# Optimization experiments

Hardware: AMD Instinct MI355X
Metric: run time of the kernel (lower is better)

Reference implementation:

```python
import jax, jax.numpy as jnp
import numpy as np

T, B, E, H = 2048, 2, 1024, 16
DH = E // H
SCALE = DH ** -0.5
NEG = jnp.finfo(jnp.float32).min


def setup_inputs() -> dict:
    key = jax.random.key(0)
    ks = jax.random.split(key, 10)
    s = 0.02
    query = jax.random.normal(ks[0], (T, B, E), dtype=jnp.float32)
    key_padding_mask = jax.random.randint(ks[1], (B, T), 0, 2).astype(bool)
    # causal additive mask, broadcastable over (bsz, heads, tgt, src)
    causal = jnp.triu(jnp.ones((T, T), dtype=bool), k=1)
    attn_mask = jnp.where(causal, NEG, 0.0).astype(jnp.float32)[None, None]
    Wq = jax.random.normal(ks[2], (E, E), jnp.float32) * s
    bq = jax.random.normal(ks[3], (E,), jnp.float32) * s
    Wk = jax.random.normal(ks[4], (E, E), jnp.float32) * s
    bk = jax.random.normal(ks[5], (E,), jnp.float32) * s
    Wv = jax.random.normal(ks[6], (E, E), jnp.float32) * s
    bv = jax.random.normal(ks[7], (E,), jnp.float32) * s
    Wo = jax.random.normal(ks[8], (E, E), jnp.float32) * s
    bo = jax.random.normal(ks[9], (E,), jnp.float32) * s
    return {"query": query, "key_padding_mask": key_padding_mask, "attn_mask": attn_mask,
            "Wq": Wq, "bq": bq, "Wk": Wk, "bk": bk, "Wv": Wv, "bv": bv, "Wo": Wo, "bo": bo}


def _heads(x):
    # [T, B, E] -> [B, H, T, DH]
    return x.reshape(T, B, H, DH).transpose(1, 2, 0, 3)


def reference(query, key_padding_mask, attn_mask, Wq, bq, Wk, bk, Wv, bv, Wo, bo):
    # projections (torch Linear: x @ W.T + b); q scaled as in module
    q = _heads((query @ Wq.T + bq) * SCALE)          # [B,H,T,DH]
    k = _heads(query @ Wk.T + bk)                    # [B,H,S,DH] (self-attn: S=T)
    v = _heads(query @ Wv.T + bv)
    scores = jnp.einsum('bhtd,bhsd->bhts', q, k)     # [B,H,T,S]
    scores = scores + attn_mask                      # additive causal mask
    # key_padding_mask True -> masked_fill with dtype min
    scores = jnp.where(key_padding_mask[:, None, None, :], NEG, scores)
    probs = jax.nn.softmax(scores, axis=-1)
    ctx = jnp.einsum('bhts,bhsd->bhtd', probs, v)    # [B,H,T,DH]
    ctx = ctx.transpose(2, 0, 1, 3).reshape(T, B, E) # back to [T,B,E]
    return ctx @ Wo.T + bo
```

## Files before the change

kernel.cpp:

```cpp
#include <hip/hip_runtime.h>
#include <hip/hip_bf16.h>
#include <stdint.h>

typedef unsigned short u16;
typedef uint32_t u32;
typedef unsigned long long u64;
typedef __attribute__((ext_vector_type(8))) short bf16x8;
typedef __attribute__((ext_vector_type(4))) float f32x4;
typedef __attribute__((ext_vector_type(16))) float f32x16;
typedef __attribute__((ext_vector_type(2))) unsigned int u32x2;
typedef __attribute__((ext_vector_type(4))) u32 u32x4;

#define T_SEQ 2048

__device__ __forceinline__ float bf2f(u16 u) {
  union { u32 i; float f; } v; v.i = ((u32)u) << 16; return v.f;
}
__device__ __forceinline__ u16 f2bf(float f) {
  union { float f; u32 i; } v; v.f = f;
  u32 u = v.i;
  return (u16)((u + 0x7fffu + ((u >> 16) & 1u)) >> 16);
}

#if __has_builtin(__builtin_amdgcn_exp2f)
#define EXP2F(x) __builtin_amdgcn_exp2f(x)
#else
#define EXP2F(x) exp2f(x)
#endif

__device__ __forceinline__ u32 permpack(float lo, float hi) {
#if __has_builtin(__builtin_amdgcn_perm)
  return __builtin_amdgcn_perm(__float_as_uint(hi), __float_as_uint(lo), 0x07060302u);
#else
  return (__float_as_uint(hi) & 0xFFFF0000u) | (__float_as_uint(lo) >> 16);
#endif
}

__device__ __forceinline__ void plswap(u32& a, u32& b) {
#if __has_builtin(__builtin_amdgcn_permlane32_swap)
  u32x2 r = __builtin_amdgcn_permlane32_swap(a, b, false, false);
  a = r[0]; b = r[1];
#else
  u32 ra = __shfl_xor(a, 32, 64), rb = __shfl_xor(b, 32, 64);
  const bool hi_ = (threadIdx.x & 32) != 0;
  u32 na = hi_ ? rb : a;
  u32 nb = hi_ ? b : ra;
  a = na; b = nb;
#endif
}
__device__ __forceinline__ float othhalf(float x, bool ishi) {
  u32 a = __float_as_uint(x), b = a;
  plswap(a, b);
  return __uint_as_float(ishi ? a : b);
}

__device__ __forceinline__ void gload_lds16(const void* g, void* l) {
  __builtin_amdgcn_global_load_lds(
      (const __attribute__((address_space(1))) void*)g,
      (__attribute__((address_space(3))) void*)l, 16, 0, 0);
}

__global__ __launch_bounds__(256) void cvt5_kernel(
    const float* __restrict__ qsrc, const float* __restrict__ w0,
    const float* __restrict__ w1, const float* __restrict__ w2,
    const float* __restrict__ w3, u16* __restrict__ qbf, u16* __restrict__ wbf) {
  const int bx = blockIdx.x;
  const float* src; u16* dst; int i;
  if (bx < 4096) {
    src = qsrc; dst = qbf; i = (bx*256 + threadIdx.x)*4;
  } else {
    int t = bx - 4096;
    int z = t >> 10;
    src = (z == 0) ? w0 : (z == 1) ? w1 : (z == 2) ? w2 : w3;
    dst = wbf + (size_t)z * 1048576;
    i = ((t & 1023)*256 + threadIdx.x)*4;
  }
  const float4 v = *(const float4*)(src + i);
  ushort4 o;
  o.x = f2bf(v.x); o.y = f2bf(v.y); o.z = f2bf(v.z); o.w = f2bf(v.w);
  *(ushort4*)(dst + i) = o;
}

__device__ __forceinline__ void gemm_core_128x128(
    f32x4 acc[2][4], const u16* __restrict__ A, const u16* __restrict__ Bw,
    int bm, int bn, u16* As, u16* Bs)
{
  const int tid = threadIdx.x;
  const int w = tid >> 6, lane = tid & 63, g = lane >> 4, c = lane & 15;
  const int wr = (w & 3) * 32, wc = (w >> 2) * 64;
  for (int k0 = 0; k0 < 1024; k0 += 64) {
    __syncthreads();
    #pragma unroll
    for (int is = 0; is < 2; ++is) {
      int o = (is*8 + w)*1024 + lane*16;
      int row = o >> 7, c16 = (o >> 4) & 7;
      gload_lds16(A + (size_t)(bm*128 + row)*1024 + k0 + (c16 ^ (row & 7))*8,
                  (char*)As + (is*8 + w)*1024);
    }
    #pragma unroll
    for (int is = 0; is < 2; ++is) {
      int o = (is*8 + w)*1024 + lane*16;
      int row = o >> 7, c16 = (o >> 4) & 7;
      gload_lds16(Bw + (size_t)(bn*128 + row)*1024 + k0 + (c16 ^ (row & 7))*8,
                  (char*)Bs + (is*8 + w)*1024);
    }
    __syncthreads();
    bf16x8 af[2][2], bfr[4][2];
    #pragma unroll
    for (int mf = 0; mf < 2; ++mf)
      #pragma unroll
      for (int kc = 0; kc < 2; ++kc) {
        int row = wr + mf*16 + c;
        int colb = kc*64 + g*16;
        af[mf][kc] = *(const bf16x8*)((const char*)As + row*128 + (colb ^ ((row & 7) << 4)));
      }
    #pragma unroll
    for (int nf = 0; nf < 4; ++nf)
      #pragma unroll
      for (int kc = 0; kc < 2; ++kc) {
        int row = wc + nf*16 + c;
        int colb = kc*64 + g*16;
        bfr[nf][kc] = *(const bf16x8*)((const char*)Bs + row*128 + (colb ^ ((row & 7) << 4)));
      }
    #pragma unroll
    for (int mf = 0; mf < 2; ++mf)
      #pragma unroll
      for (int nf = 0; nf < 4; ++nf)
        #pragma unroll
        for (int kc = 0; kc < 2; ++kc)
          acc[mf][nf] = __builtin_amdgcn_mfma_f32_16x16x32_bf16(
              af[mf][kc], bfr[nf][kc], acc[mf][nf], 0, 0, 0);
  }
}

__global__ __launch_bounds__(512, 2) void gemm_qkv(
    const u16* __restrict__ Abf, const u16* __restrict__ Wbf,
    const float* __restrict__ bq, const float* __restrict__ bk,
    const float* __restrict__ bv, u16* __restrict__ qkvh)
{
  __shared__ __align__(16) u16 As[128*64];
  __shared__ __align__(16) u16 Bs[128*64];
  f32x4 acc[2][4];
  #pragma unroll
  for (int mf = 0; mf < 2; ++mf)
    #pragma unroll
    for (int nf = 0; nf < 4; ++nf) acc[mf][nf] = (f32x4){0.f,0.f,0.f,0.f};
  const int bx = blockIdx.x;
  const int bm = (bx & 7) * 4 + (bx >> 3);
  gemm_core_128x128(acc, Abf, Wbf, bm, blockIdx.y, As, Bs);
  const int tid = threadIdx.x, w = tid >> 6, lane = tid & 63, g = lane >> 4, c = lane & 15;
  const int wr = (w & 3) * 32, wc = (w >> 2) * 64;
  #pragma unroll
  for (int mf = 0; mf < 2; ++mf)
    #pragma unroll
    for (int nf = 0; nf < 4; ++nf) {
      int col = blockIdx.y*128 + wc + nf*16 + c;
      int z = col >> 10, colz = col & 1023;
      const float* bias = (z == 0) ? bq : (z == 1) ? bk : bv;
      float bcol = bias[colz];
      float scl = (z == 0) ? 0.18033688011112043f : 1.0f;
      int h = colz >> 6, d = colz & 63;
      u16* dst = qkvh + (size_t)z * 4194304;
      #pragma unroll
      for (int r = 0; r < 4; ++r) {
        int row = bm*128 + wr + mf*16 + g*4 + r;
        int t = row >> 1, bb = row & 1;
        float v = (acc[mf][nf][r] + bcol) * scl;
        dst[(size_t)(bb*16 + h)*131072 + (size_t)t*64 + d] = f2bf(v);
      }
    }
}

__global__ __launch_bounds__(512, 2) void gemm_out(
    const u16* __restrict__ ctx2, const u16* __restrict__ Wobf,
    const float* __restrict__ bo, float* __restrict__ out)
{
  __shared__ __align__(16) u16 As[128*64];
  __shared__ __align__(16) u16 Bs[128*64];
  f32x4 acc[2][4];
  #pragma unroll
  for (int mf = 0; mf < 2; ++mf)
    #pragma unroll
    for (int nf = 0; nf < 4; ++nf) acc[mf][nf] = (f32x4){0.f,0.f,0.f,0.f};
  const int bx = blockIdx.x;
  const int bm = (bx & 7) * 4 + (bx >> 3);
  gemm_core_128x128(acc, ctx2, Wobf, bm, blockIdx.y, As, Bs);
  const int tid = threadIdx.x, w = tid >> 6, lane = tid & 63, g = lane >> 4, c = lane & 15;
  const int wr = (w & 3) * 32, wc = (w >> 2) * 64;
  #pragma unroll
  for (int mf = 0; mf < 2; ++mf)
    #pragma unroll
    for (int nf = 0; nf < 4; ++nf) {
      int col = blockIdx.y*128 + wc + nf*16 + c;
      float bcol = bo[col];
      #pragma unroll
      for (int r = 0; r < 4; ++r) {
        int row = bm*128 + wr + mf*16 + g*4 + r;
        out[(size_t)row*1024 + col] = acc[mf][nf][r] + bcol;
      }
    }
}

__global__ __launch_bounds__(256) void vtrans_kernel(const u16* __restrict__ Vh,
                                                     u16* __restrict__ Vt,
                                                     float* __restrict__ vs) {
  __shared__ u16 tile[64][72];
  const int bh = blockIdx.x >> 5, tc = blockIdx.x & 31;
  const int t0 = tc * 64;
  const int tid = threadIdx.x;
  {
    const int tl = tid >> 2, d0 = (tid & 3) * 16;
    const u16* src = Vh + (size_t)bh*131072 + (size_t)(t0 + tl)*64 + d0;
    bf16x8 a = *(const bf16x8*)src;
    bf16x8 b2 = *(const bf16x8*)(src + 8);
    #pragma unroll
    for (int j = 0; j < 8; ++j) {
      tile[d0 + j][tl] = (u16)a[j];
      tile[d0 + 8 + j][tl] = (u16)b2[j];
    }
  }
  __syncthreads();
  {
    const int d = tid >> 2, tq = (tid & 3) * 16;
    bf16x8 o0, o1;
    float s = 0.f;
    #pragma unroll
    for (int j = 0; j < 8; ++j) {
      u16 x0 = tile[d][tq + j], x1 = tile[d][tq + 8 + j];
      o0[j] = (short)x0; o1[j] = (short)x1;
      s += bf2f(x0) + bf2f(x1);
    }
    u16* dst = Vt + (size_t)bh*131072 + (size_t)d*2048 + t0 + tq;
    *(bf16x8*)dst = o0;
    *(bf16x8*)(dst + 8) = o1;
    s += __shfl_xor(s, 1, 64);
    s += __shfl_xor(s, 2, 64);
    if ((tid & 3) == 0) atomicAdd(&vs[bh*64 + d], s);
  }
}

#define ZERO16 (f32x16){0.f,0.f,0.f,0.f,0.f,0.f,0.f,0.f,0.f,0.f,0.f,0.f,0.f,0.f,0.f,0.f}
#define NEGINF (-__builtin_inff())

__device__ const unsigned char CTBL[40] = {
  60, 44, 28, 12, 57, 59, 52, 37,
  61, 45, 29, 42, 40, 56, 53, 38,
  62, 46, 24, 25, 41, 58, 54, 49,
  63,  8, 20, 21, 32, 34, 55, 51,
   0,  4, 16, 17, 33, 36, 48, 50 };

__device__ __forceinline__ int pctx_off(int k, int ch) {
  if (k < 8)  return (k - 4);
  if (k < 12) return 4 + (k - 8)*2 + (ch - 1);
  return 12 + (k - 12)*3 + (ch - 1);
}
__device__ __forceinline__ int pml_off(int k, int ch) {
  if (k < 8)  return (k - 4)*2 + ch;
  if (k < 12) return 8 + (k - 8)*3 + ch;
  return 20 + (k - 12)*4 + ch;
}

__global__ __launch_bounds__(256, 2) void flash_attn(
    const u16* __restrict__ Qh, const u16* __restrict__ Kh,
    const u16* __restrict__ Vt, const int* __restrict__ kpm,
    const float* __restrict__ vsum, u16* __restrict__ ctx2,
    u16* __restrict__ pctxA, u16* __restrict__ pctxB,
    float* __restrict__ pml)
{
  __shared__ __align__(16) u16 Kl[2][4096];
  __shared__ __align__(16) u16 Vl[2][4096];

  const int tid = threadIdx.x;
  const int w = tid >> 6, lane = tid & 63;
  const int l31 = lane & 31, hi = lane >> 5;

  const int id = blockIdx.x;
  const int xcd = id & 7, rest = id >> 3;
  const int bh = xcd * 4 + (rest & 3);
  const int cidx = rest >> 2;
  const int v_tbl = CTBL[cidx];
  const int k = v_tbl >> 2, ch = v_tbl & 3;
  const int NS = (k >> 2) + 1;
  const int nt = 2*k + 2;
  const int lo = (nt * ch) / NS, hicap = (nt * (ch + 1)) / NS;

  const int b = bh >> 4, h = bh & 15;
  const size_t hbase = (size_t)bh * 131072;
  const int q = 128*k + 32*w + l31;
  const int myNt = 2*k + 1 + (w >> 1);

  bf16x8 qfrag[4];
  #pragma unroll
  for (int kt = 0; kt < 4; ++kt)
    qfrag[kt] = *(const bf16x8*)(Qh + hbase + (size_t)q*64 + kt*16 + hi*8);

  {
    const int s0t = lo * 64;
    const int jb = (w & 1) * 4;
    if (w < 2) {
      #pragma unroll
      for (int is = 0; is < 4; ++is) {
        int o = (jb + is)*1024 + lane*16;
        int row = o >> 7, c16 = (o >> 4) & 7;
        gload_lds16(Kh + hbase + (size_t)(s0t + row)*64 + (c16 ^ (row & 7))*8,
                    (char*)Kl[0] + (jb + is)*1024);
      }
    } else {
      #pragma unroll
      for (int is = 0; is < 4; ++is) {
        int o = (jb + is)*1024 + lane*16;
        int row = o >> 7, c16 = (o >> 4) & 7;
        gload_lds16(Vt + hbase + (size_t)row*2048 + s0t + (c16 ^ (row & 7))*8,
                    (char*)Vl[0] + (jb + is)*1024);
      }
    }
  }
  int kpmv_cur = kpm[b*T_SEQ + lo*64 + lane];
  int kpmv_nxt = 0;
  __syncthreads();

  float mrow = NEGINF, lrow = 0.f;
  f32x16 cacc0 = ZERO16, cacc1 = ZERO16;

  for (int t = lo; t < hicap; ++t) {
    const int cur = (t - lo) & 1, nxt = cur ^ 1;
    const int s0 = t * 64;
    const bool notLast = (t + 1 < hicap);
    const bool diag = (t >= myNt - 1);

    if (notLast) {
      const int s0n = s0 + 64;
      const int jb = (w & 1) * 4;
      if (w < 2) {
        #pragma unroll
        for (int is = 0; is < 4; ++is) {
          int o = (jb + is)*1024 + lane*16;
          int row = o >> 7, c16 = (o >> 4) & 7;
          gload_lds16(Kh + hbase + (size_t)(s0n + row)*64 + (c16 ^ (row & 7))*8,
                      (char*)Kl[nxt] + (jb + is)*1024);
        }
      } else {
        #pragma unroll
        for (int is = 0; is < 4; ++is) {
          int o = (jb + is)*1024 + lane*16;
          int row = o >> 7, c16 = (o >> 4) & 7;
          gload_lds16(Vt + hbase + (size_t)row*2048 + s0n + (c16 ^ (row & 7))*8,
                      (char*)Vl[nxt] + (jb + is)*1024);
        }
      }
      kpmv_nxt = kpm[b*T_SEQ + s0n + lane];
    }

    u32 kill0 = 0, kill1 = 0;
    {
      const u64 mask = __ballot(kpmv_cur != 0);
      const u32 m0 = (u32)mask, m1 = (u32)(mask >> 32);
      const u64 m4 = mask >> 4;
      const u32 m4l = (u32)m4, m4h = (u32)(m4 >> 32);
      const u32 w0m = hi ? m4l : m0;
      const u32 w1m = hi ? m4h : m1;
      const int lim = q - s0 - 4*hi;
      #pragma unroll
      for (int m = 0; m < 4; ++m) {
        u32 nib0 = (w0m >> (m*8)) & 15u;
        u32 nib1 = (w1m >> (m*8)) & 15u;
        if (diag) {
          int t0c = lim - m*8;       int c0 = min(max(t0c + 1, 0), 4);
          int t1c = lim - 32 - m*8;  int c1 = min(max(t1c + 1, 0), 4);
          nib0 |= (0xFu << c0) & 0xFu;
          nib1 |= (0xFu << c1) & 0xFu;
        }
        kill0 |= nib0 << (m*4);
        kill1 |= nib1 << (m*4);
      }
    }
    f32x16 st0, st1;
    #pragma unroll
    for (int i = 0; i < 16; ++i) {
      st0[i] = ((kill0 >> i) & 1u) ? NEGINF : 0.f;
      st1[i] = ((kill1 >> i) & 1u) ? NEGINF : 0.f;
    }

    bf16x8 kreg[2][4], vf[2][4];
    #pragma unroll
    for (int sub = 0; sub < 2; ++sub)
      #pragma unroll
      for (int kt = 0; kt < 4; ++kt) {
        int row = sub*32 + l31;
        int colb = kt*32 + hi*16;
        kreg[sub][kt] = *(const bf16x8*)((const char*)Kl[cur] + row*128 + (colb ^ ((row & 7) << 4)));
        vf[sub][kt]   = *(const bf16x8*)((const char*)Vl[cur] + row*128 + (colb ^ ((row & 7) << 4)));
      }

    __builtin_amdgcn_s_setprio(1);
    #pragma unroll
    for (int kt = 0; kt < 4; ++kt) {
      st0 = __builtin_amdgcn_mfma_f32_32x32x16_bf16(kreg[0][kt], qfrag[kt], st0, 0, 0, 0);
      st1 = __builtin_amdgcn_mfma_f32_32x32x16_bf16(kreg[1][kt], qfrag[kt], st1, 0, 0, 0);
    }
    __builtin_amdgcn_s_setprio(0);

    {
      float t8[8];
      #pragma unroll
      for (int i = 0; i < 8; ++i)
        t8[i] = fmaxf(fmaxf(st0[i], st0[i+8]), fmaxf(st1[i], st1[i+8]));
      float t4a = fmaxf(t8[0], t8[4]), t4b = fmaxf(t8[1], t8[5]);
      float t4c = fmaxf(t8[2], t8[6]), t4d = fmaxf(t8[3], t8[7]);
      float rm = fmaxf(fmaxf(t4a, t4b), fmaxf(t4c, t4d));
      rm = fmaxf(rm, othhalf(rm, hi != 0));

      const bool need = (rm > mrow + 8.f) || (mrow < -1e30f);
      if (__any(need)) {
        const float mn = fmaxf(mrow, rm);
        const float sc = (mn < -1e30f) ? 1.f : EXP2F(mrow - mn);
        mrow = mn;
        lrow *= sc;
        #pragma unroll
        for (int i = 0; i < 16; ++i) { cacc0[i] *= sc; cacc1[i] *= sc; }
      }
      const bool dead = (mrow < -1e30f);
      float a0 = 0.f, a1 = 0.f, a2 = 0.f, a3 = 0.f;
      #pragma unroll
      for (int i = 0; i < 16; i += 4) {
        float p0 = dead ? 0.f : EXP2F(st0[i+0] - mrow); st0[i+0] = p0; a0 += p0;
        float p1 = dead ? 0.f : EXP2F(st0[i+1] - mrow); st0[i+1] = p1; a1 += p1;
        float p2 = dead ? 0.f : EXP2F(st0[i+2] - mrow); st0[i+2] = p2; a2 += p2;
        float p3 = dead ? 0.f : EXP2F(st0[i+3] - mrow); st0[i+3] = p3; a3 += p3;
      }
      #pragma unroll
      for (int i = 0; i < 16; i += 4) {
        float p0 = dead ? 0.f : EXP2F(st1[i+0] - mrow); st1[i+0] = p0; a0 += p0;
        float p1 = dead ? 0.f : EXP2F(st1[i+1] - mrow); st1[i+1] = p1; a1 += p1;
        float p2 = dead ? 0.f : EXP2F(st1[i+2] - mrow); st1[i+2] = p2; a2 += p2;
        float p3 = dead ? 0.f : EXP2F(st1[i+3] - mrow); st1[i+3] = p3; a3 += p3;
      }
      float ps = (a0 + a1) + (a2 + a3);
      ps += othhalf(ps, hi != 0);
      lrow += ps;
    }

    u32 pk[8][2];
    #pragma unroll
    for (int m = 0; m < 4; ++m) {
      pk[m][0]   = permpack(st0[m*4+0], st0[m*4+1]);
      pk[m][1]   = permpack(st0[m*4+2], st0[m*4+3]);
      pk[4+m][0] = permpack(st1[m*4+0], st1[m*4+1]);
      pk[4+m][1] = permpack(st1[m*4+2], st1[m*4+3]);
    }
    bf16x8 pf[4];
    #pragma unroll
    for (int ks = 0; ks < 4; ++ks) {
      u32 w0p = pk[2*ks][0], w2p = pk[2*ks+1][0];
      u32 w1p = pk[2*ks][1], w3p = pk[2*ks+1][1];
      plswap(w0p, w2p);
      plswap(w1p, w3p);
      u32x4 wv = {w0p, w1p, w2p, w3p};
      pf[ks] = __builtin_bit_cast(bf16x8, wv);
    }

    __builtin_amdgcn_s_setprio(1);
    #pragma unroll
    for (int ks = 0; ks < 4; ++ks)
      cacc0 = __builtin_amdgcn_mfma_f32_32x32x16_bf16(vf[0][ks], pf[ks], cacc0, 0, 0, 0);
    #pragma unroll
    for (int ks = 0; ks < 4; ++ks)
      cacc1 = __builtin_amdgcn_mfma_f32_32x32x16_bf16(vf[1][ks], pf[ks], cacc1, 0, 0, 0);
    __builtin_amdgcn_s_setprio(0);

    kpmv_cur = kpmv_nxt;
    if (notLast) __syncthreads();
  }

  if (NS == 1) {
    const bool dead = (lrow == 0.f);
    const float rl = dead ? 0.f : 1.f / lrow;
    #pragma unroll
    for (int subd = 0; subd < 2; ++subd) {
      #pragma unroll
      for (int m = 0; m < 4; ++m) {
        const int d0 = subd*32 + hi*4 + m*8;
        float v0 = (subd ? cacc1[m*4+0] : cacc0[m*4+0]) * rl;
        float v1 = (subd ? cacc1[m*4+1] : cacc0[m*4+1]) * rl;
        float v2 = (subd ? cacc1[m*4+2] : cacc0[m*4+2]) * rl;
        float v3 = (subd ? cacc1[m*4+3] : cacc0[m*4+3]) * rl;
        if (dead) {
          const float* vs = vsum + bh*64 + d0;
          v0 = vs[0] * (1.0f/2048.0f);
          v1 = vs[1] * (1.0f/2048.0f);
          v2 = vs[2] * (1.0f/2048.0f);
          v3 = vs[3] * (1.0f/2048.0f);
        }
        ushort4 o;
        o.x = f2bf(v0); o.y = f2bf(v1); o.z = f2bf(v2); o.w = f2bf(v3);
        *(ushort4*)(ctx2 + (size_t)(q*2 + b)*1024 + h*64 + d0) = o;
      }
    }
  } else {
    const int row = w*32 + l31;
    if (!hi) {
      float2 ml; ml.x = mrow; ml.y = lrow;
      *(float2*)(pml + (size_t)(bh*36 + pml_off(k, ch))*256 + row*2) = ml;
    }
    u16* pc;
    if (ch == 0) {
      pc = ctx2 + (size_t)(q*2 + b)*1024 + h*64;
    } else {
      const int slot = bh*24 + pctx_off(k, ch);
      pc = (slot < 512) ? (pctxA + (size_t)slot*8192)
                        : (pctxB + (size_t)(slot - 512)*8192);
      pc += (size_t)row*64;
    }
    #pragma unroll
    for (int subd = 0; subd < 2; ++subd) {
      #pragma unroll
      for (int m = 0; m < 4; ++m) {
        const int d0 = subd*32 + hi*4 + m*8;
        const f32x16& cc = subd ? cacc1 : cacc0;
        ushort4 o;
        o.x = f2bf(cc[m*4+0]); o.y = f2bf(cc[m*4+1]);
        o.z = f2bf(cc[m*4+2]); o.w = f2bf(cc[m*4+3]);
        *(ushort4*)(pc + d0) = o;
      }
    }
  }
}

__global__ __launch_bounds__(256) void combine_kernel(
    const u16* __restrict__ pctxA, const u16* __restrict__ pctxB,
    const float* __restrict__ pml, const float* __restrict__ vsum,
    u16* __restrict__ ctx2)
{
  const int k = 4 + blockIdx.x;
  const int bh = blockIdx.y;
  const int NS = (k >> 2) + 1;
  const int b = bh >> 4, h = bh & 15;
  const int tid = threadIdx.x;
  const int row = tid >> 1, dh = (tid & 1) * 32;
  const int q = k*128 + row;

  const float* mlb = pml + (size_t)(bh*36 + pml_off(k, 0))*256 + row*2;
  float m0v = mlb[0],        l0v = mlb[1];
  float m1v = mlb[256+0],    l1v = mlb[256+1];
  float m2v = NEGINF, l2v = 0.f, m3v = NEGINF, l3v = 0.f;
  if (NS > 2) { m2v = mlb[512+0];  l2v = mlb[512+1]; }
  if (NS > 3) { m3v = mlb[768+0];  l3v = mlb[768+1]; }
  float ms = fmaxf(fmaxf(m0v, m1v), fmaxf(m2v, m3v));
  bool dead = (ms < -1e30f);
  const float w0 = dead ? 0.f : EXP2F(m0v - ms);
  const float w1 = dead ? 0.f : EXP2F(m1v - ms);
  const float w2 = (dead || NS <= 2) ? 0.f : EXP2F(m2v - ms);
  const float w3 = (dead || NS <= 3) ? 0.f : EXP2F(m3v - ms);
  const float lt = w0*l0v + w1*l1v + w2*l2v + w3*l3v;
  dead = dead || (lt == 0.f);
  const float rl = dead ? 0.f : 1.f / lt;

  u16* dst = ctx2 + (size_t)(q*2 + b)*1024 + h*64 + dh;
  const u16* pc1; const u16* pc2 = nullptr; const u16* pc3 = nullptr;
  {
    const int s1 = bh*24 + pctx_off(k, 1);
    pc1 = ((s1 < 512) ? (pctxA + (size_t)s1*8192) : (pctxB + (size_t)(s1-512)*8192))
          + (size_t)row*64 + dh;
    if (NS > 2) {
      const int s2 = bh*24 + pctx_off(k, 2);
      pc2 = ((s2 < 512) ? (pctxA + (size_t)s2*8192) : (pctxB + (size_t)(s2-512)*8192))
            + (size_t)row*64 + dh;
    }
    if (NS > 3) {
      const int s3 = bh*24 + pctx_off(k, 3);
      pc3 = ((s3 < 512) ? (pctxA + (size_t)s3*8192) : (pctxB + (size_t)(s3-512)*8192))
            + (size_t)row*64 + dh;
    }
  }
  #pragma unroll
  for (int g2 = 0; g2 < 4; ++g2) {
    bf16x8 a0 = *(const bf16x8*)(dst + g2*8);
    bf16x8 a1 = *(const bf16x8*)(pc1 + g2*8);
    bf16x8 o;
    #pragma unroll
    for (int j = 0; j < 8; ++j) {
      float v = w0*bf2f((u16)a0[j]) + w1*bf2f((u16)a1[j]);
      if (NS > 2) v += w2*bf2f((u16)((const u16*)pc2)[g2*8 + j]);
      if (NS > 3) v += w3*bf2f((u16)((const u16*)pc3)[g2*8 + j]);
      v *= rl;
      if (dead) v = vsum[bh*64 + dh + g2*8 + j] * (1.0f/2048.0f);
      o[j] = (short)f2bf(v);
    }
    *(bf16x8*)(dst + g2*8) = o;
  }
}

extern "C" void kernel_launch(void* const* d_in, const int* in_sizes, int n_in,
                              void* d_out, int out_size, void* d_ws, size_t ws_size,
                              hipStream_t stream) {
  const float* query = (const float*)d_in[0];
  const int*   kpm   = (const int*)d_in[1];
  const float* Wq = (const float*)d_in[3];
  const float* bq = (const float*)d_in[4];
  const float* Wk = (const float*)d_in[5];
  const float* bk = (const float*)d_in[6];
  const float* Wv = (const float*)d_in[7];
  const float* bv = (const float*)d_in[8];
  const float* Wo = (const float*)d_in[9];
  const float* bo = (const float*)d_in[10];

  char* ws = (char*)d_ws;
  u16*   qbf   = (u16*)(ws);
  u16*   Vt    = (u16*)(ws);
  u16*   wbf   = (u16*)(ws + 8388608);
  u16*   pctxB = (u16*)(ws + 8388608);
  u16*   qkvh  = (u16*)(ws + 16777216);
  u16*   pctxA = (u16*)(ws + 33554432);
  u16*   ctx2  = (u16*)(ws + 41943040);
  float* vsum  = (float*)(ws + 50331648);
  float* pml   = (float*)(ws + 50339840);

  cvt5_kernel<<<dim3(8192), 256, 0, stream>>>(query, Wq, Wk, Wv, Wo, qbf, wbf);

  hipMemsetAsync(vsum, 0, 2048 * sizeof(float), stream);

  gemm_qkv<<<dim3(32, 24), 512, 0, stream>>>(qbf, wbf, bq, bk, bv, qkvh);
  vtrans_kernel<<<dim3(1024), 256, 0, stream>>>(qkvh + 2*4194304, Vt, vsum);
  flash_attn<<<dim3(1280), 256, 0, stream>>>(qkvh, qkvh + 1*4194304,
                                             Vt, kpm, vsum, ctx2, pctxA, pctxB, pml);
  combine_kernel<<<dim3(12, 32), 256, 0, stream>>>(pctxA, pctxB, pml, vsum, ctx2);
  gemm_out<<<dim3(32, 8), 512, 0, stream>>>(ctx2, wbf + 3*1048576, bo, (float*)d_out);
}
```

Before: 141.8 us.

## Deepen flash-attention K/V prefetch to two tiles and precompute padding-mask bitmasks

The attention loop now keeps two K/V tiles in flight. It prefetches tile t+2 into the buffer just consumed and waits with explicit vmcnt counts and raw barriers instead of a full __syncthreads after issuing loads. The key-padding mask is packed into 64-bit ballot words by an extra block in the conversion kernel, so each attention iteration reads one u64 instead of a per-lane int load plus a ballot. This aims to hide global-load latency more fully and drop per-tile mask work. It relies on precise hand-written waitcnt values, which is fragile if the compiler reorders or adds memory ops.

```diff
diff --git a/kernel.cpp b/kernel.cpp
--- a/kernel.cpp
+++ b/kernel.cpp
@@ -63,8 +63,18 @@
 __global__ __launch_bounds__(256) void cvt5_kernel(
     const float* __restrict__ qsrc, const float* __restrict__ w0,
     const float* __restrict__ w1, const float* __restrict__ w2,
-    const float* __restrict__ w3, u16* __restrict__ qbf, u16* __restrict__ wbf) {
+    const float* __restrict__ w3, const int* __restrict__ kpm,
+    u16* __restrict__ qbf, u16* __restrict__ wbf, u64* __restrict__ kpmbits) {
   const int bx = blockIdx.x;
+  if (bx == 8192) {
+    const int wv = threadIdx.x >> 6, lane = threadIdx.x & 63;
+    for (int pair = wv; pair < 64; pair += 4) {
+      int v = kpm[pair*64 + lane];
+      u64 m = __ballot(v != 0);
+      if (lane == 0) kpmbits[pair] = m;
+    }
+    return;
+  }
   const float* src; u16* dst; int i;
   if (bx < 4096) {
     src = qsrc; dst = qbf; i = (bx*256 + threadIdx.x)*4;
@@ -262,7 +272,7 @@
 
 __global__ __launch_bounds__(256, 2) void flash_attn(
     const u16* __restrict__ Qh, const u16* __restrict__ Kh,
-    const u16* __restrict__ Vt, const int* __restrict__ kpm,
+    const u16* __restrict__ Vt, const u64* __restrict__ kpmbits,
     const float* __restrict__ vsum, u16* __restrict__ ctx2,
     u16* __restrict__ pctxA, u16* __restrict__ pctxB,
     float* __restrict__ pml)
@@ -294,9 +304,11 @@
   for (int kt = 0; kt < 4; ++kt)
     qfrag[kt] = *(const bf16x8*)(Qh + hbase + (size_t)q*64 + kt*16 + hi*8);
 
+  const int jb = (w & 1) * 4;
+
+  u64 mcur = kpmbits[(b << 5) + lo];
   {
     const int s0t = lo * 64;
-    const int jb = (w & 1) * 4;
     if (w < 2) {
       #pragma unroll
       for (int is = 0; is < 4; ++is) {
@@ -315,47 +327,45 @@
       }
     }
   }
-  int kpmv_cur = kpm[b*T_SEQ + lo*64 + lane];
-  int kpmv_nxt = 0;
-  __syncthreads();
+  if (lo + 1 < hicap) {
+    const int s0t = (lo + 1) * 64;
+    if (w < 2) {
+      #pragma unroll
+      for (int is = 0; is < 4; ++is) {
+        int o = (jb + is)*1024 + lane*16;
+        int row = o >> 7, c16 = (o >> 4) & 7;
+        gload_lds16(Kh + hbase + (size_t)(s0t + row)*64 + (c16 ^ (row & 7))*8,
+                    (char*)Kl[1] + (jb + is)*1024);
+      }
+    } else {
+      #pragma unroll
+      for (int is = 0; is < 4; ++is) {
+        int o = (jb + is)*1024 + lane*16;
+        int row = o >> 7, c16 = (o >> 4) & 7;
+        gload_lds16(Vt + hbase + (size_t)row*2048 + s0t + (c16 ^ (row & 7))*8,
+                    (char*)Vl[1] + (jb + is)*1024);
+      }
+    }
+  }
 
   float mrow = NEGINF, lrow = 0.f;
   f32x16 cacc0 = ZERO16, cacc1 = ZERO16;
 
   for (int t = lo; t < hicap; ++t) {
-    const int cur = (t - lo) & 1, nxt = cur ^ 1;
+    const int cur = (t - lo) & 1;
     const int s0 = t * 64;
-    const bool notLast = (t + 1 < hicap);
+    const bool haveNext = (t + 1 < hicap);
     const bool diag = (t >= myNt - 1);
 
-    if (notLast) {
-      const int s0n = s0 + 64;
-      const int jb = (w & 1) * 4;
-      if (w < 2) {
-        #pragma unroll
-        for (int is = 0; is < 4; ++is) {
-          int o = (jb + is)*1024 + lane*16;
-          int row = o >> 7, c16 = (o >> 4) & 7;
-          gload_lds16(Kh + hbase + (size_t)(s0n + row)*64 + (c16 ^ (row & 7))*8,
-                      (char*)Kl[nxt] + (jb + is)*1024);
-        }
-      } else {
-        #pragma unroll
-        for (int is = 0; is < 4; ++is) {
-          int o = (jb + is)*1024 + lane*16;
-          int row = o >> 7, c16 = (o >> 4) & 7;
-          gload_lds16(Vt + hbase + (size_t)row*2048 + s0n + (c16 ^ (row & 7))*8,
-                      (char*)Vl[nxt] + (jb + is)*1024);
-        }
-      }
-      kpmv_nxt = kpm[b*T_SEQ + s0n + lane];
-    }
+    if (haveNext) asm volatile("s_waitcnt vmcnt(4)" ::: "memory");
+    else          asm volatile("s_waitcnt vmcnt(0)" ::: "memory");
+    u64 mnxt = haveNext ? kpmbits[(b << 5) + t + 1] : 0;
+    __builtin_amdgcn_s_barrier();
 
     u32 kill0 = 0, kill1 = 0;
     {
-      const u64 mask = __ballot(kpmv_cur != 0);
-      const u32 m0 = (u32)mask, m1 = (u32)(mask >> 32);
-      const u64 m4 = mask >> 4;
+      const u32 m0 = (u32)mcur, m1 = (u32)(mcur >> 32);
+      const u64 m4 = mcur >> 4;
       const u32 m4l = (u32)m4, m4h = (u32)(m4 >> 32);
       const u32 w0m = hi ? m4l : m0;
       const u32 w1m = hi ? m4h : m1;
@@ -468,8 +478,28 @@
       cacc1 = __builtin_amdgcn_mfma_f32_32x32x16_bf16(vf[1][ks], pf[ks], cacc1, 0, 0, 0);
     __builtin_amdgcn_s_setprio(0);
 
-    kpmv_cur = kpmv_nxt;
-    if (notLast) __syncthreads();
+    __builtin_amdgcn_s_barrier();
+    if (t + 2 < hicap) {
+      const int s0n = (t + 2) * 64;
+      if (w < 2) {
+        #pragma unroll
+        for (int is = 0; is < 4; ++is) {
+          int o = (jb + is)*1024 + lane*16;
+          int row = o >> 7, c16 = (o >> 4) & 7;
+          gload_lds16(Kh + hbase + (size_t)(s0n + row)*64 + (c16 ^ (row & 7))*8,
+                      (char*)Kl[cur] + (jb + is)*1024);
+        }
+      } else {
+        #pragma unroll
+        for (int is = 0; is < 4; ++is) {
+          int o = (jb + is)*1024 + lane*16;
+          int row = o >> 7, c16 = (o >> 4) & 7;
+          gload_lds16(Vt + hbase + (size_t)row*2048 + s0n + (c16 ^ (row & 7))*8,
+                      (char*)Vl[cur] + (jb + is)*1024);
+        }
+      }
+    }
+    mcur = mnxt;
   }
 
   if (NS == 1) {
@@ -605,24 +635,27 @@
   const float* bo = (const float*)d_in[10];
 
   char* ws = (char*)d_ws;
-  u16*   qbf   = (u16*)(ws);
-  u16*   Vt    = (u16*)(ws);
-  u16*   wbf   = (u16*)(ws + 8388608);
-  u16*   pctxB = (u16*)(ws + 8388608);
-  u16*   qkvh  = (u16*)(ws + 16777216);
-  u16*   pctxA = (u16*)(ws + 33554432);
-  u16*   ctx2  = (u16*)(ws + 41943040);
-  float* vsum  = (float*)(ws + 50331648);
-  float* pml   = (float*)(ws + 50339840);
-
-  cvt5_kernel<<<dim3(8192), 256, 0, stream>>>(query, Wq, Wk, Wv, Wo, qbf, wbf);
+  u16*   qbf     = (u16*)(ws);
+  u16*   Vt      = (u16*)(ws);
+  u16*   wbf     = (u16*)(ws + 8388608);
+  u16*   pctxB   = (u16*)(ws + 8388608);
+  u16*   qkvh    = (u16*)(ws + 16777216);
+  u16*   pctxA   = (u16*)(ws + 33554432);
+  u16*   ctx2    = (u16*)(ws + 41943040);
+  float* vsum    = (float*)(ws + 50331648);
+  float* pml     = (float*)(ws + 50339840);
+  u64*   kpmbits = (u64*)(ws + 51650560);
+
+  cvt5_kernel<<<dim3(8193), 256, 0, stream>>>(query, Wq, Wk, Wv, Wo, kpm,
+                                              qbf, wbf, kpmbits);
 
   hipMemsetAsync(vsum, 0, 2048 * sizeof(float), stream);
 
   gemm_qkv<<<dim3(32, 24), 512, 0, stream>>>(qbf, wbf, bq, bk, bv, qkvh);
   vtrans_kernel<<<dim3(1024), 256, 0, stream>>>(qkvh + 2*4194304, Vt, vsum);
   flash_attn<<<dim3(1280), 256, 0, stream>>>(qkvh, qkvh + 1*4194304,
-                                             Vt, kpm, vsum, ctx2, pctxA, pctxB, pml);
+                                             Vt, kpmbits, vsum, ctx2,
+                                             pctxA, pctxB, pml);
   combine_kernel<<<dim3(12, 32), 256, 0, stream>>>(pctxA, pctxB, pml, vsum, ctx2);
   gemm_out<<<dim3(32, 8), 512, 0, stream>>>(ctx2, wbf + 3*1048576, bo, (float*)d_out);
 }
```

After: 143.9 us. Within noise of the previous version (+1.5%).
